# Optimization experiments

Measured on AMD Instinct MI355X. Metric: run time of the kernel, lower is better.

## Reference

```python
import jax, jax.numpy as jnp
import numpy as np

B, N, DIM, PDIM, H, DH, M, CDIM = 1, 48, 256, 128, 8, 64, 128, 512
INNER = H * DH
EPS = 1e-5


def setup_inputs() -> dict:
    key = jax.random.key(0)
    ks = jax.random.split(key, 40)
    def w(k, shape):
        return jax.random.normal(k, shape, jnp.float32) * 0.02
    inp = {
        "singles": jax.random.normal(ks[0], (B, N, DIM), jnp.float32),
        "pairs": jax.random.normal(ks[1], (B, N, N, PDIM), jnp.float32),
        "ligand_emb": jax.random.normal(ks[2], (B, M, CDIM), jnp.float32),
        "mask": jnp.ones((B, N), dtype=bool),
        "rotary_pos": jax.random.normal(ks[3], (1, 1, 1, DH), jnp.float32),
        "ln_s_g": jnp.ones((DIM,)), "ln_s_b": jnp.zeros((DIM,)),
        "ln_p_g": jnp.ones((PDIM,)), "ln_p_b": jnp.zeros((PDIM,)),
        "sa_qkv": w(ks[4], (DIM, 3 * INNER)),
        "sa_out_w": w(ks[5], (INNER, DIM)), "sa_out_b": jnp.zeros((DIM,)),
        "sff_w1": w(ks[6], (DIM, 4 * DIM)), "sff_b1": jnp.zeros((4 * DIM,)),
        "sff_w2": w(ks[7], (4 * DIM, DIM)), "sff_b2": jnp.zeros((DIM,)),
        "pa_qkv": w(ks[8], (PDIM, 3 * INNER)),
        "pa_out_w": w(ks[9], (INNER, PDIM)), "pa_out_b": jnp.zeros((PDIM,)),
        "pff_w1": w(ks[10], (PDIM, 4 * PDIM)), "pff_b1": jnp.zeros((4 * PDIM,)),
        "pff_w2": w(ks[11], (4 * PDIM, PDIM)), "pff_b2": jnp.zeros((PDIM,)),
        "ca_q": w(ks[12], (PDIM, INNER)),
        "ca_kv": w(ks[13], (CDIM, 2 * INNER)),
        "ca_out_w": w(ks[14], (INNER, PDIM)), "ca_out_b": jnp.zeros((PDIM,)),
        "s2p_w": w(ks[15], (DIM, PDIM)), "s2p_b": jnp.zeros((PDIM,)),
        "p2s_w": w(ks[16], (PDIM, DIM)), "p2s_b": jnp.zeros((DIM,)),
    }
    return inp


def _rotate_half(x):
    shp = x.shape
    xr = x.reshape(shp[:-1] + (shp[-1] // 2, 2))
    x1, x2 = xr[..., 0], xr[..., 1]
    return jnp.stack((-x2, x1), axis=-1).reshape(shp)


def _rope(pos, t):
    return t * jnp.cos(pos) + _rotate_half(t) * jnp.sin(pos)


def _split_heads(t):
    b, n, _ = t.shape
    return t.reshape(b, n, H, DH).transpose(0, 2, 1, 3)  # b h n d


def _merge_heads(t):
    b, h, n, d = t.shape
    return t.transpose(0, 2, 1, 3).reshape(b, n, h * d)


def _layer_norm(x, g, b):
    m = jnp.mean(x, axis=-1, keepdims=True)
    v = jnp.mean(jnp.square(x - m), axis=-1, keepdims=True)
    return (x - m) * jax.lax.rsqrt(v + EPS) * g + b


def _mish(x):
    return x * jnp.tanh(jax.nn.softplus(x))


def _attn_core(q, k, v, key_mask=None):
    dots = jnp.einsum('bhid,bhjd->bhij', q, k) * (DH ** -0.5)
    if key_mask is not None:
        neg = -jnp.finfo(dots.dtype).max
        dots = jnp.where(key_mask[:, None, None, :], dots, neg)
    a = jax.nn.softmax(dots, axis=-1)
    return jnp.einsum('bhij,bhjd->bhid', a, v)


def _self_attn(x, w_qkv, w_out, b_out, rotary_pos, key_mask=None):
    q, k, v = jnp.split(x @ w_qkv, 3, axis=-1)
    q, k, v = _split_heads(q), _split_heads(k), _split_heads(v)
    q, k = _rope(rotary_pos, q), _rope(rotary_pos, k)
    out = _merge_heads(_attn_core(q, k, v, key_mask))
    return out @ w_out + b_out


def _cross_attn(x, ctx, w_q, w_kv, w_out, b_out, rotary_pos):
    q = _split_heads(x @ w_q)
    k, v = jnp.split(ctx @ w_kv, 2, axis=-1)
    k, v = _split_heads(k), _split_heads(v)
    q, k = _rope(rotary_pos, q), _rope(rotary_pos, k)
    out = _merge_heads(_attn_core(q, k, v))
    return out @ w_out + b_out


def _ff(x, w1, b1, w2, b2):
    return _mish(x @ w1 + b1) @ w2 + b2


def _forward(singles, pairs, ligand_emb, mask, rotary_pos,
             ln_s_g, ln_s_b, ln_p_g, ln_p_b,
             sa_qkv, sa_out_w, sa_out_b, sff_w1, sff_b1, sff_w2, sff_b2,
             pa_qkv, pa_out_w, pa_out_b, pff_w1, pff_b1, pff_w2, pff_b2,
             ca_q, ca_kv, ca_out_w, ca_out_b, s2p_w, s2p_b, p2s_w, p2s_b):
    # single track
    s_norm = _layer_norm(singles, ln_s_g, ln_s_b)
    singles = singles + _self_attn(s_norm, sa_qkv, sa_out_w, sa_out_b, rotary_pos, mask)
    singles = singles + _ff(singles, sff_w1, sff_b1, sff_w2, sff_b2)
    # pair track: flatten i*j into one long sequence
    b, i, j, d = pairs.shape
    p_norm = _layer_norm(pairs, ln_p_g, ln_p_b)
    p_flat = p_norm.reshape(b, i * j, d)
    p_attn = _self_attn(p_flat, pa_qkv, pa_out_w, pa_out_b, rotary_pos, None)
    pairs = pairs + p_attn.reshape(b, i, j, d)
    # ligand cross attention (on pre-norm pairs, as in source)
    p_cross = _cross_attn(p_flat, ligand_emb, ca_q, ca_kv, ca_out_w, ca_out_b, rotary_pos)
    pairs = pairs + p_cross.reshape(b, i, j, d)
    pairs = pairs + _ff(pairs, pff_w1, pff_b1, pff_w2, pff_b2)
    # cross-track communication
    single_contrib = singles @ s2p_w + s2p_b              # [b,n,pdim]
    pair_contrib = jnp.mean(pairs, axis=2) @ p2s_w + p2s_b  # [b,n,dim]
    pairs = pairs + single_contrib[:, None, :, :] + single_contrib[:, :, None, :]
    singles = singles + pair_contrib
    return singles, pairs


def reference(singles, pairs, ligand_emb, mask, rotary_pos,
              ln_s_g, ln_s_b, ln_p_g, ln_p_b,
              sa_qkv, sa_out_w, sa_out_b, sff_w1, sff_b1, sff_w2, sff_b2,
              pa_qkv, pa_out_w, pa_out_b, pff_w1, pff_b1, pff_w2, pff_b2,
              ca_q, ca_kv, ca_out_w, ca_out_b, s2p_w, s2p_b, p2s_w, p2s_b):
    return _forward(singles, pairs, ligand_emb, mask, rotary_pos,
                    ln_s_g, ln_s_b, ln_p_g, ln_p_b,
                    sa_qkv, sa_out_w, sa_out_b, sff_w1, sff_b1, sff_w2, sff_b2,
                    pa_qkv, pa_out_w, pa_out_b, pff_w1, pff_b1, pff_w2, pff_b2,
                    ca_q, ca_kv, ca_out_w, ca_out_b, s2p_w, s2p_b, p2s_w, p2s_b)
```

## Files before the change

### kernel.cpp

```cpp
#include <hip/hip_runtime.h>
#include <math.h>

#define EPS 1e-5f

typedef __attribute__((ext_vector_type(8))) short short8;
typedef __attribute__((ext_vector_type(4))) short short4v;
typedef __attribute__((ext_vector_type(4))) float float4v;

__device__ inline short f2bf(float f) {
  union { float f; unsigned u; } c; c.f = f;
  unsigned u = c.u;
  u += 0x7FFF + ((u >> 16) & 1);
  return (short)(u >> 16);
}
__device__ inline float bf2f(short s) {
  union { unsigned u; float f; } c;
  c.u = ((unsigned)(unsigned short)s) << 16;
  return c.f;
}

__global__ __launch_bounds__(256) void ln_kernel(
    const float* __restrict__ xs, const float* __restrict__ gs,
    const float* __restrict__ bs, float* __restrict__ ys,
    const float* __restrict__ xp, const float* __restrict__ gp,
    const float* __restrict__ bp, float* __restrict__ yp) {
  const float *x, *g, *b;
  float* y;
  int D, row;
  if (blockIdx.x < 48) {
    row = blockIdx.x; x = xs; g = gs; b = bs; y = ys; D = 256;
  } else {
    row = blockIdx.x - 48; x = xp; g = gp; b = bp; y = yp; D = 128;
  }
  const float* xr = x + (size_t)row * D;
  float* yr = y + (size_t)row * D;
  __shared__ float red[256];
  int tid = threadIdx.x;
  float s = (tid < D) ? xr[tid] : 0.f;
  red[tid] = s; __syncthreads();
  for (int st = 128; st > 0; st >>= 1) {
    if (tid < st) red[tid] += red[tid + st];
    __syncthreads();
  }
  float mean = red[0] / D;
  __syncthreads();
  float v = 0.f;
  if (tid < D) { float t = xr[tid] - mean; v = t * t; }
  red[tid] = v; __syncthreads();
  for (int st = 128; st > 0; st >>= 1) {
    if (tid < st) red[tid] += red[tid + st];
    __syncthreads();
  }
  float rstd = rsqrtf(red[0] / D + EPS);
  if (tid < D) yr[tid] = (xr[tid] - mean) * rstd * g[tid] + b[tid];
}

struct TransDesc { const float* src; short* dst; int K; int N; int tile0; };
struct TransArgs { TransDesc d[13]; int nd; };

__global__ __launch_bounds__(256) void transpose_weights_kernel(TransArgs args) {
  int t = blockIdx.x;
  int wi = 0;
  while (wi + 1 < args.nd && args.d[wi + 1].tile0 <= t) ++wi;
  TransDesc de = args.d[wi];
  int lt = t - de.tile0;
  int ntx = de.N / 32;
  int k0 = (lt / ntx) * 32, n0 = (lt % ntx) * 32;
  __shared__ float tile[32][33];
  int tx = threadIdx.x & 31, ty = threadIdx.x >> 5;
#pragma unroll
  for (int yy = 0; yy < 4; ++yy) {
    int kk = ty + yy * 8;
    tile[kk][tx] = de.src[(size_t)(k0 + kk) * de.N + n0 + tx];
  }
  __syncthreads();
#pragma unroll
  for (int yy = 0; yy < 4; ++yy) {
    int nn = ty + yy * 8;
    de.dst[(size_t)(n0 + nn) * de.K + k0 + tx] = f2bf(tile[tx][nn]);
  }
}

struct ProjJob {
  const float* A; const short* Wt;
  int M, K, N;
  short *Qd, *Kd, *Vd;
  int rowspad, vld, qend, kend, tile0;
  float qscale;
};
struct ProjArgs { ProjJob j[4]; int nj; };

__global__ __launch_bounds__(256) void proj_kernel(
    ProjArgs args, const float* __restrict__ rope_pos) {
  __shared__ short As[64][72];
  __shared__ short Ws[64][72];
  int t = blockIdx.x;
  int ji = 0;
  while (ji + 1 < args.nj && args.j[ji + 1].tile0 <= t) ++ji;
  ProjJob jb = args.j[ji];
  int lt = t - jb.tile0;
  int ntx = jb.N / 64;
  int m0 = (lt / ntx) * 64, n0 = (lt % ntx) * 64;
  int tid = threadIdx.x;
  int wave = tid >> 6, lane = tid & 63;
  int n16 = lane & 15, quad = lane >> 4;
  float4v acc[4];
#pragma unroll
  for (int f = 0; f < 4; ++f) acc[f] = (float4v){0.f, 0.f, 0.f, 0.f};

  for (int k0 = 0; k0 < jb.K; k0 += 64) {
    __syncthreads();
    for (int idx = tid; idx < 1024; idx += 256) {
      int row = idx >> 4, c4 = (idx & 15) * 4;
      float4 av = make_float4(0.f, 0.f, 0.f, 0.f);
      if (m0 + row < jb.M)
        av = *(const float4*)(jb.A + (size_t)(m0 + row) * jb.K + k0 + c4);
      short4v s;
      s.x = f2bf(av.x); s.y = f2bf(av.y); s.z = f2bf(av.z); s.w = f2bf(av.w);
      *(short4v*)&As[row][c4] = s;
    }
    for (int idx = tid; idx < 512; idx += 256) {
      int row = idx >> 3, kc = (idx & 7) * 8;
      short8 w = *(const short8*)(jb.Wt + (size_t)(n0 + row) * jb.K + k0 + kc);
      *(short8*)&Ws[row][kc] = w;
    }
    __syncthreads();
#pragma unroll
    for (int s = 0; s < 2; ++s) {
      short8 a = *(const short8*)&As[wave * 16 + n16][s * 32 + quad * 8];
#pragma unroll
      for (int f = 0; f < 4; ++f) {
        short8 b = *(const short8*)&Ws[f * 16 + n16][s * 32 + quad * 8];
        acc[f] = __builtin_amdgcn_mfma_f32_16x16x32_bf16(a, b, acc[f], 0, 0, 0);
      }
    }
  }

#pragma unroll
  for (int f = 0; f < 4; ++f) {
    int col = n0 + f * 16 + n16;
    if (col < jb.kend) {
      int rel = (col < jb.qend) ? col : col - jb.qend;
      int hh = rel >> 6, d = col & 63;
      float pv = rope_pos[d];
      float cp = cosf(pv), sp = sinf(pv);
      float sc = (col < jb.qend) ? jb.qscale : 1.f;
      short* dst = (col < jb.qend) ? jb.Qd : jb.Kd;
#pragma unroll
      for (int r = 0; r < 4; ++r) {
        float x = acc[f][r];
        float xp = __shfl_xor(x, 1);
        float o = (n16 & 1) ? (x * cp + xp * sp) : (x * cp - xp * sp);
        int row = m0 + wave * 16 + quad * 4 + r;
        if (row < jb.M)
          dst[((size_t)hh * jb.rowspad + row) * 64 + d] = f2bf(o * sc);
      }
    } else {
      int vcol = col - jb.kend;
      int hh = vcol >> 6, d = vcol & 63;
      short4v s;
#pragma unroll
      for (int r = 0; r < 4; ++r) ((short*)&s)[r] = f2bf(acc[f][r]);
      int j0 = m0 + wave * 16 + quad * 4;
      if (j0 < jb.M)
        *(short4v*)(jb.Vd + (size_t)(hh * 64 + d) * jb.vld + j0) = s;
    }
  }
}

struct FJob {
  const short *Q, *K, *V;
  int nkpad;
  float* O;
  short* Opart; float* Lpart;
  int nq, nk, ns, nqt, blk0;
};
struct FArgs { FJob j[3]; int nj; };

__global__ __launch_bounds__(256) void fattn_kernel(FArgs args) {
  __shared__ short Ks[64][72];
  __shared__ short Vs[64][72];
  __shared__ short Ps[4][16][72];
  int bid = blockIdx.x;
  int ji = 0;
  while (ji + 1 < args.nj && args.j[ji + 1].blk0 <= bid) ++ji;
  FJob jb = args.j[ji];
  int local = bid - jb.blk0;
  int h = local & 7;
  int rest = local >> 3;
  int qt = rest % jb.nqt;
  int z = rest / jb.nqt;
  int nqpad = jb.nqt * 64;
  int q0 = qt * 64;
  int nsplit = jb.ns;
  int nkpad = jb.nkpad, nk = jb.nk;
  int tid = threadIdx.x;
  int wave = tid >> 6, lane = tid & 63;
  int n16 = lane & 15, quad = lane >> 4;

  int ntiles = nkpad >> 6;
  int tiles_per = (ntiles + nsplit - 1) / nsplit;
  int kbeg = z * tiles_per * 64;
  int kend = min(nkpad, kbeg + tiles_per * 64);

  const short* kb = jb.K + (size_t)h * nkpad * 64;
  const short* vt = jb.V + (size_t)h * 64 * nkpad;
  const short* qr = jb.Q + (size_t)h * nqpad * 64 +
                    (size_t)(q0 + wave * 16 + n16) * 64;
  short8 a0 = *(const short8*)(qr + quad * 8);
  short8 a1 = *(const short8*)(qr + 32 + quad * 8);

  float4v Of[4];
#pragma unroll
  for (int f = 0; f < 4; ++f) Of[f] = (float4v){0.f, 0.f, 0.f, 0.f};
  float l_par[4] = {0.f, 0.f, 0.f, 0.f};

  int r0 = tid >> 3, cc0 = (tid & 7) * 8;
  int r1 = (tid + 256) >> 3, cc1 = ((tid + 256) & 7) * 8;

  short8 pK0 = *(const short8*)(kb + (size_t)(kbeg + r0) * 64 + cc0);
  short8 pK1 = *(const short8*)(kb + (size_t)(kbeg + r1) * 64 + cc1);
  short8 pV0 = *(const short8*)(vt + (size_t)r0 * nkpad + kbeg + cc0);
  short8 pV1 = *(const short8*)(vt + (size_t)r1 * nkpad + kbeg + cc1);

  for (int kt0 = kbeg; kt0 < kend; kt0 += 64) {
    __syncthreads();
    *(short8*)&Ks[r0][cc0] = pK0;
    *(short8*)&Ks[r1][cc1] = pK1;
    *(short8*)&Vs[r0][cc0] = pV0;
    *(short8*)&Vs[r1][cc1] = pV1;
    int nxt = kt0 + 64;
    if (nxt < kend) {
      pK0 = *(const short8*)(kb + (size_t)(nxt + r0) * 64 + cc0);
      pK1 = *(const short8*)(kb + (size_t)(nxt + r1) * 64 + cc1);
      pV0 = *(const short8*)(vt + (size_t)r0 * nkpad + nxt + cc0);
      pV1 = *(const short8*)(vt + (size_t)r1 * nkpad + nxt + cc1);
    }
    __syncthreads();

    float4v Sf[4];
#pragma unroll
    for (int f = 0; f < 4; ++f) {
      short8 b0 = *(const short8*)&Ks[f * 16 + n16][quad * 8];
      short8 b1 = *(const short8*)&Ks[f * 16 + n16][32 + quad * 8];
      float4v a = (float4v){0.f, 0.f, 0.f, 0.f};
      a = __builtin_amdgcn_mfma_f32_16x16x32_bf16(a0, b0, a, 0, 0, 0);
      a = __builtin_amdgcn_mfma_f32_16x16x32_bf16(a1, b1, a, 0, 0, 0);
      Sf[f] = a;
    }
    if (kt0 + 64 > nk) {
#pragma unroll
      for (int f = 0; f < 4; ++f) {
        int j = kt0 + f * 16 + n16;
        if (j >= nk) {
          Sf[f][0] = -1e30f; Sf[f][1] = -1e30f;
          Sf[f][2] = -1e30f; Sf[f][3] = -1e30f;
        }
      }
    }
    float p[4][4];
#pragma unroll
    for (int r = 0; r < 4; ++r) {
      float t = 0.f;
#pragma unroll
      for (int f = 0; f < 4; ++f) {
        float e = __expf(Sf[f][r]);
        p[f][r] = e;
        t += e;
      }
      l_par[r] += t;
    }
#pragma unroll
    for (int f = 0; f < 4; ++f)
#pragma unroll
      for (int r = 0; r < 4; ++r)
        Ps[wave][quad * 4 + r][f * 16 + n16] = f2bf(p[f][r]);
#pragma unroll
    for (int s = 0; s < 2; ++s) {
      short8 pa = *(const short8*)&Ps[wave][n16][s * 32 + quad * 8];
#pragma unroll
      for (int f = 0; f < 4; ++f) {
        short8 vb = *(const short8*)&Vs[f * 16 + n16][s * 32 + quad * 8];
        Of[f] = __builtin_amdgcn_mfma_f32_16x16x32_bf16(pa, vb, Of[f], 0, 0, 0);
      }
    }
  }

  float l[4];
#pragma unroll
  for (int r = 0; r < 4; ++r) {
    float t = l_par[r];
    t += __shfl_xor(t, 1);
    t += __shfl_xor(t, 2);
    t += __shfl_xor(t, 4);
    t += __shfl_xor(t, 8);
    l[r] = t;
  }

  if (nsplit == 1) {
#pragma unroll
    for (int r = 0; r < 4; ++r) {
      int row = q0 + wave * 16 + quad * 4 + r;
      if (row >= jb.nq) continue;
      float inv = 1.f / l[r];
#pragma unroll
      for (int f = 0; f < 4; ++f)
        jb.O[(size_t)row * 512 + h * 64 + f * 16 + n16] = Of[f][r] * inv;
    }
  } else {
    size_t pbase = ((size_t)(h * jb.nqt + qt) * nsplit + z);
    short* op = jb.Opart + pbase * 4096;
#pragma unroll
    for (int r = 0; r < 4; ++r) {
      int rl = wave * 16 + quad * 4 + r;
#pragma unroll
      for (int f = 0; f < 4; ++f)
        op[(size_t)rl * 64 + f * 16 + n16] = f2bf(Of[f][r]);
      if (n16 == 0) jb.Lpart[pbase * 64 + rl] = l[r];
    }
  }
}

__global__ __launch_bounds__(256) void attn_combine_kernel(
    const short* __restrict__ Opart, const float* __restrict__ Lpart,
    float* __restrict__ O, int os, int nsplit) {
  int h = blockIdx.x, qt = blockIdx.y;
  int tid = threadIdx.x;
  int q = tid >> 2, d0 = (tid & 3) * 16;
  size_t base = (size_t)(h * gridDim.y + qt) * nsplit;
  float l = 0.f;
  for (int s = 0; s < nsplit; ++s) l += Lpart[(base + s) * 64 + q];
  float inv = 1.f / l;
  float acc[16];
#pragma unroll
  for (int i = 0; i < 16; ++i) acc[i] = 0.f;
  for (int s = 0; s < nsplit; ++s) {
    const short* op = Opart + (base + s) * 4096 + q * 64 + d0;
#pragma unroll
    for (int c = 0; c < 2; ++c) {
      short8 v = *(const short8*)(op + c * 8);
#pragma unroll
      for (int j = 0; j < 8; ++j) acc[c * 8 + j] += bf2f(v[j]);
    }
  }
  int row = qt * 64 + q;
  float* dst = O + (size_t)row * os + h * 64 + d0;
#pragma unroll
  for (int c = 0; c < 4; ++c) {
    float4 o = make_float4(acc[c * 4] * inv, acc[c * 4 + 1] * inv,
                           acc[c * 4 + 2] * inv, acc[c * 4 + 3] * inv);
    *(float4*)(dst + c * 4) = o;
  }
}

struct TJob {
  int type;
  const float *A1, *A2;
  const short *W1, *W2;
  const float *b1, *b2, *resid;
  float* C;
  int M, Kseg, N, nz, dual, mish, tile0;
};
struct TArgs { TJob j[2]; int nj; };

__global__ __launch_bounds__(256) void tjobs_kernel(TArgs args) {
  __shared__ short As[32][136];
  __shared__ short Ws[32][136];
  int t = blockIdx.x;
  int ji = 0;
  while (ji + 1 < args.nj && args.j[ji + 1].tile0 <= t) ++ji;
  TJob jb = args.j[ji];
  int lt = t - jb.tile0;
  int tid = threadIdx.x;

  if (jb.type == 1) {
    int i = lt;
    if (tid < 128) {
      float acc = 0.f;
      for (int j = 0; j < 48; ++j)
        acc += jb.A1[((size_t)i * 48 + j) * 128 + tid];
      jb.C[i * 128 + tid] = acc * (1.f / 48.f);
    }
    return;
  }
  if (jb.type == 2) {
    int idx = lt * 256 + tid;
    int d = idx & 127;
    int j = (idx >> 7) % 48;
    int i = idx / (48 * 128);
    jb.C[idx] = jb.A1[idx] + jb.A2[j * 128 + d] + jb.A2[i * 128 + d];
    return;
  }

  int ntx = jb.N / 32, nmt = (jb.M + 31) >> 5;
  int per_z = ntx * nmt;
  int z = lt / per_z, rem = lt - z * per_z;
  int m0 = (rem / ntx) * 32, n0 = (rem % ntx) * 32;
  int wave = tid >> 6, lane = tid & 63;
  int n16 = lane & 15, quad = lane >> 4;
  int mrow = (wave >> 1) * 16, ncol = (wave & 1) * 16;
  float4v acc = (float4v){0.f, 0.f, 0.f, 0.f};
  int Ktot = jb.dual ? 2 * jb.Kseg : jb.Kseg;
  int chunk = Ktot / jb.nz;
  int kst = z * chunk, ken = kst + chunk;
  for (int kc = kst; kc < ken; kc += 128) {
    __syncthreads();
    for (int idx = tid; idx < 1024; idx += 256) {
      int row = idx >> 5, c4 = (idx & 31) * 4;
      int k = kc + c4;
      float4 av = make_float4(0.f, 0.f, 0.f, 0.f);
      if (m0 + row < jb.M) {
        const float* src = (jb.dual && k >= jb.Kseg)
            ? (jb.A2 + (size_t)(m0 + row) * jb.Kseg + (k - jb.Kseg))
            : (jb.A1 + (size_t)(m0 + row) * jb.Kseg + k);
        av = *(const float4*)src;
      }
      short4v s;
      s.x = f2bf(av.x); s.y = f2bf(av.y); s.z = f2bf(av.z); s.w = f2bf(av.w);
      *(short4v*)&As[row][c4] = s;
    }
    for (int idx = tid; idx < 512; idx += 256) {
      int row = idx >> 4, k8 = (idx & 15) * 8;
      int k = kc + k8;
      const short* src = (jb.dual && k >= jb.Kseg)
          ? (jb.W2 + (size_t)(n0 + row) * jb.Kseg + (k - jb.Kseg))
          : (jb.W1 + (size_t)(n0 + row) * jb.Kseg + k);
      *(short8*)&Ws[row][k8] = *(const short8*)src;
    }
    __syncthreads();
#pragma unroll
    for (int ks = 0; ks < 4; ++ks) {
      short8 a = *(const short8*)&As[mrow + n16][ks * 32 + quad * 8];
      short8 b = *(const short8*)&Ws[ncol + n16][ks * 32 + quad * 8];
      acc = __builtin_amdgcn_mfma_f32_16x16x32_bf16(a, b, acc, 0, 0, 0);
    }
  }
  int col = n0 + ncol + n16;
  if (jb.nz == 1) {
#pragma unroll
    for (int r = 0; r < 4; ++r) {
      int row = m0 + mrow + quad * 4 + r;
      if (row >= jb.M) continue;
      float v = acc[r] + jb.b1[col];
      if (jb.dual) v += jb.b2[col];
      if (jb.mish) {
        float sp = (v > 20.f) ? v : log1pf(expf(v));
        v = v * tanhf(sp);
      }
      if (jb.resid) v += jb.resid[(size_t)row * jb.N + col];
      jb.C[(size_t)row * jb.N + col] = v;
    }
  } else {
#pragma unroll
    for (int r = 0; r < 4; ++r) {
      int row = m0 + mrow + quad * 4 + r;
      if (row >= jb.M) continue;
      float v = acc[r];
      if (z == 0) {
        v += jb.b1[col];
        if (jb.dual) v += jb.b2[col];
        if (jb.resid) v += jb.resid[(size_t)row * jb.N + col];
      }
      atomicAdd(&jb.C[(size_t)row * jb.N + col], v);
    }
  }
}

extern "C" void kernel_launch(void* const* d_in, const int* in_sizes, int n_in,
                              void* d_out, int out_size, void* d_ws, size_t ws_size,
                              hipStream_t stream) {
  (void)in_sizes; (void)n_in; (void)out_size; (void)ws_size;
  const float* singles = (const float*)d_in[0];
  const float* pairs   = (const float*)d_in[1];
  const float* ligand  = (const float*)d_in[2];
  const float* rotary  = (const float*)d_in[4];
  const float* ln_s_g  = (const float*)d_in[5];
  const float* ln_s_b  = (const float*)d_in[6];
  const float* ln_p_g  = (const float*)d_in[7];
  const float* ln_p_b  = (const float*)d_in[8];
  const float* sa_out_b= (const float*)d_in[11];
  const float* sff_b1  = (const float*)d_in[13];
  const float* sff_b2  = (const float*)d_in[15];
  const float* pa_out_b= (const float*)d_in[18];
  const float* pff_b1  = (const float*)d_in[20];
  const float* pff_b2  = (const float*)d_in[22];
  const float* ca_out_b= (const float*)d_in[26];
  const float* s2p_b   = (const float*)d_in[28];
  const float* p2s_b   = (const float*)d_in[30];

  float* ws = (float*)d_ws;
  size_t off = 0;
  auto alloc = [&](size_t n) { float* p = ws + off; off += n; return p; };
  float* s_norm   = alloc(12288);
  float* p_norm   = alloc(294912);
  float* attn_s   = alloc(24576);
  float* h1_s     = alloc(49152);
  float* attn_p   = alloc(294912);
  float* attn_c   = alloc(1179648);
  float* pairs2   = alloc(294912);
  float* pairs3   = alloc(294912);
  float* singles1 = alloc(12288);
  float* singles2 = alloc(12288);
  float* sc_buf   = alloc(6144);
  size_t zero_floats = 294912 * 2 + 12288 * 2 + 6144;
  float* pmean    = alloc(6144);
  float* Lpart    = alloc(73728);
  short* OpartS   = (short*)alloc(2359296);
  short* wt       = (short*)alloc(1081344);
  short* Qb       = (short*)alloc(589824);
  short* Kb       = (short*)alloc(589824);
  short* Vtb      = (short*)alloc(589824);
  short* Qcb      = (short*)alloc(589824);
  short* Kcb      = (short*)alloc(32768);
  short* Vcb      = (short*)alloc(32768);
  short* Qsb      = (short*)alloc(16384);
  short* Ksb      = (short*)alloc(16384);
  short* Vsb      = (short*)alloc(16384);

  float* out_s = (float*)d_out;
  float* out_p = (float*)d_out + 12288;

  struct WSpec { const float* src; int K, N; };
  WSpec specs[13] = {
    {(const float*)d_in[9], 256, 1536}, {(const float*)d_in[10], 512, 256},
    {(const float*)d_in[12], 256, 1024}, {(const float*)d_in[14], 1024, 256},
    {(const float*)d_in[16], 128, 1536}, {(const float*)d_in[17], 512, 128},
    {(const float*)d_in[19], 128, 512}, {(const float*)d_in[21], 512, 128},
    {(const float*)d_in[23], 128, 512}, {(const float*)d_in[24], 512, 1024},
    {(const float*)d_in[25], 512, 128}, {(const float*)d_in[27], 256, 128},
    {(const float*)d_in[29], 128, 256}};
  TransArgs ta;
  ta.nd = 13;
  short* wptr[13];
  int tiles = 0;
  size_t woff = 0;
  for (int i = 0; i < 13; ++i) {
    ta.d[i].src = specs[i].src;
    ta.d[i].dst = wt + woff;
    ta.d[i].K = specs[i].K;
    ta.d[i].N = specs[i].N;
    ta.d[i].tile0 = tiles;
    wptr[i] = wt + woff;
    woff += (size_t)specs[i].K * specs[i].N;
    tiles += (specs[i].K / 32) * (specs[i].N / 32);
  }
  hipLaunchKernelGGL(transpose_weights_kernel, dim3(tiles), dim3(256), 0,
                     stream, ta);
  hipMemsetAsync(pairs2, 0, zero_floats * sizeof(float), stream);

  const float scale = 0.125f;
  const int NS = 4;

  hipLaunchKernelGGL(ln_kernel, dim3(48 + 2304), dim3(256), 0, stream,
                     singles, ln_s_g, ln_s_b, s_norm,
                     pairs, ln_p_g, ln_p_b, p_norm);

  {
    ProjArgs pa;
    pa.nj = 4;
    int t0 = 0;
    auto setj = [&](int i, const float* A, const short* Wt, int M, int K,
                    int N, short* Qd, short* Kd, short* Vd, int rowspad,
                    int vld, int qend, int kend, float qscale) {
      pa.j[i] = {A, Wt, M, K, N, Qd, Kd, Vd, rowspad, vld, qend, kend, t0,
                 qscale};
      t0 += (N / 64) * ((M + 63) / 64);
    };
    setj(0, s_norm, wptr[0], 48, 256, 1536, Qsb, Ksb, Vsb, 64, 64, 512, 1024,
         scale);
    setj(1, p_norm, wptr[4], 2304, 128, 1536, Qb, Kb, Vtb, 2304, 2304, 512,
         1024, scale);
    setj(2, p_norm, wptr[8], 2304, 128, 512, Qcb, nullptr, nullptr, 2304, 0,
         512, 512, scale);
    setj(3, ligand, wptr[9], 128, 512, 1024, nullptr, Kcb, Vcb, 128, 128, 0,
         512, 1.f);
    hipLaunchKernelGGL(proj_kernel, dim3(t0), dim3(256), 0, stream, pa, rotary);
  }

  {
    FArgs fa;
    fa.nj = 3;
    fa.j[0] = {Qb, Kb, Vtb, 2304, attn_p, OpartS, Lpart, 2304, 2304, NS, 36, 0};
    fa.j[1] = {Qsb, Ksb, Vsb, 64, attn_s, nullptr, nullptr, 48, 48, 1, 1,
               8 * 36 * NS};
    fa.j[2] = {Qcb, Kcb, Vcb, 128, attn_c, nullptr, nullptr, 2304, 128, 1, 36,
               8 * 36 * NS + 8};
    int nblk = 8 * 36 * NS + 8 + 8 * 36;
    hipLaunchKernelGGL(fattn_kernel, dim3(nblk), dim3(256), 0, stream, fa);
  }

  hipLaunchKernelGGL(attn_combine_kernel, dim3(8, 36), dim3(256), 0, stream,
                     OpartS, Lpart, attn_p, 512, NS);

  auto launch_tjobs = [&](TJob a, TJob b, int nb) {
    TArgs tj;
    tj.nj = 2;
    tj.j[0] = a;
    tj.j[1] = b;
    hipLaunchKernelGGL(tjobs_kernel, dim3(nb), dim3(256), 0, stream, tj);
  };
  auto gemm_tiles = [](int M, int N, int nz) {
    return (N / 32) * ((M + 31) / 32) * nz;
  };

  {
    TJob a = {0, attn_p, attn_c, wptr[5], wptr[10], pa_out_b, ca_out_b, pairs,
              pairs2, 2304, 512, 128, 4, 1, 0, 0};
    int t1 = gemm_tiles(2304, 128, 4);
    TJob b = {0, attn_s, nullptr, wptr[1], nullptr, sa_out_b, nullptr, singles,
              singles1, 48, 512, 256, 2, 0, 0, t1};
    launch_tjobs(a, b, t1 + gemm_tiles(48, 256, 2));
  }
  {
    TJob a = {0, pairs2, nullptr, wptr[6], nullptr, pff_b1, nullptr, nullptr,
              attn_c , 2304, 128, 512, 1, 0, 1, 0};
    int t1 = gemm_tiles(2304, 512, 1);
    TJob b = {0, singles1, nullptr, wptr[2], nullptr, sff_b1, nullptr, nullptr,
              h1_s, 48, 256, 1024, 1, 0, 1, t1};
    launch_tjobs(a, b, t1 + gemm_tiles(48, 1024, 1));
  }
  {
    TJob a = {0, attn_c , nullptr, wptr[7], nullptr, pff_b2, nullptr,
              pairs2, pairs3, 2304, 512, 128, 2, 0, 0, 0};
    int t1 = gemm_tiles(2304, 128, 2);
    TJob b = {0, h1_s, nullptr, wptr[3], nullptr, sff_b2, nullptr, singles1,
              singles2, 48, 1024, 256, 2, 0, 0, t1};
    launch_tjobs(a, b, t1 + gemm_tiles(48, 256, 2));
  }
  {
    TJob a = {0, singles2, nullptr, wptr[11], nullptr, s2p_b, nullptr, nullptr,
              sc_buf, 48, 256, 128, 2, 0, 0, 0};
    int t1 = gemm_tiles(48, 128, 2);
    TJob b = {1, pairs3, nullptr, nullptr, nullptr, nullptr, nullptr, nullptr,
              pmean, 0, 0, 0, 1, 0, 0, t1};
    launch_tjobs(a, b, t1 + 48);
  }
  {
    TJob a = {0, pmean, nullptr, wptr[12], nullptr, p2s_b, nullptr, singles2,
              out_s, 48, 128, 256, 1, 0, 0, 0};
    int t1 = gemm_tiles(48, 256, 1);
    TJob b = {2, pairs3, sc_buf, nullptr, nullptr, nullptr, nullptr, nullptr,
              out_p, 0, 0, 0, 1, 0, 0, t1};
    launch_tjobs(a, b, t1 + 1152);
  }
}
```

Before: 239.4 us.

## Fuse prep kernels, replace split-K combine with atomics, fold s2p into FF

Measured after the change: 288.9 us. 20.7% more time.

```diff
diff --git a/kernel.cpp b/kernel.cpp
--- a/kernel.cpp
+++ b/kernel.cpp
@@ -13,72 +13,72 @@
   u += 0x7FFF + ((u >> 16) & 1);
   return (short)(u >> 16);
 }
-__device__ inline float bf2f(short s) {
-  union { unsigned u; float f; } c;
-  c.u = ((unsigned)(unsigned short)s) << 16;
-  return c.f;
-}
-
-__global__ __launch_bounds__(256) void ln_kernel(
+
+struct TransDesc { const float* src; short* dst; int K; int N; int tile0; };
+struct TransArgs { TransDesc d[13]; int nd; };
+
+__global__ __launch_bounds__(256) void prep_kernel(
+    TransArgs args, int tiles, int ln_end,
     const float* __restrict__ xs, const float* __restrict__ gs,
     const float* __restrict__ bs, float* __restrict__ ys,
     const float* __restrict__ xp, const float* __restrict__ gp,
-    const float* __restrict__ bp, float* __restrict__ yp) {
-  const float *x, *g, *b;
-  float* y;
-  int D, row;
-  if (blockIdx.x < 48) {
-    row = blockIdx.x; x = xs; g = gs; b = bs; y = ys; D = 256;
-  } else {
-    row = blockIdx.x - 48; x = xp; g = gp; b = bp; y = yp; D = 128;
-  }
-  const float* xr = x + (size_t)row * D;
-  float* yr = y + (size_t)row * D;
-  __shared__ float red[256];
+    const float* __restrict__ bp, float* __restrict__ yp,
+    float* __restrict__ zbase) {
+  int bid = blockIdx.x;
   int tid = threadIdx.x;
-  float s = (tid < D) ? xr[tid] : 0.f;
-  red[tid] = s; __syncthreads();
-  for (int st = 128; st > 0; st >>= 1) {
-    if (tid < st) red[tid] += red[tid + st];
-    __syncthreads();
-  }
-  float mean = red[0] / D;
-  __syncthreads();
-  float v = 0.f;
-  if (tid < D) { float t = xr[tid] - mean; v = t * t; }
-  red[tid] = v; __syncthreads();
-  for (int st = 128; st > 0; st >>= 1) {
-    if (tid < st) red[tid] += red[tid + st];
-    __syncthreads();
-  }
-  float rstd = rsqrtf(red[0] / D + EPS);
-  if (tid < D) yr[tid] = (xr[tid] - mean) * rstd * g[tid] + b[tid];
-}
-
-struct TransDesc { const float* src; short* dst; int K; int N; int tile0; };
-struct TransArgs { TransDesc d[13]; int nd; };
-
-__global__ __launch_bounds__(256) void transpose_weights_kernel(TransArgs args) {
-  int t = blockIdx.x;
-  int wi = 0;
-  while (wi + 1 < args.nd && args.d[wi + 1].tile0 <= t) ++wi;
-  TransDesc de = args.d[wi];
-  int lt = t - de.tile0;
-  int ntx = de.N / 32;
-  int k0 = (lt / ntx) * 32, n0 = (lt % ntx) * 32;
-  __shared__ float tile[32][33];
-  int tx = threadIdx.x & 31, ty = threadIdx.x >> 5;
-#pragma unroll
-  for (int yy = 0; yy < 4; ++yy) {
-    int kk = ty + yy * 8;
-    tile[kk][tx] = de.src[(size_t)(k0 + kk) * de.N + n0 + tx];
-  }
-  __syncthreads();
-#pragma unroll
-  for (int yy = 0; yy < 4; ++yy) {
-    int nn = ty + yy * 8;
-    de.dst[(size_t)(n0 + nn) * de.K + k0 + tx] = f2bf(tile[tx][nn]);
-  }
+  if (bid < tiles) {
+    __shared__ float tile[32][33];
+    int wi = 0;
+    while (wi + 1 < args.nd && args.d[wi + 1].tile0 <= bid) ++wi;
+    TransDesc de = args.d[wi];
+    int lt = bid - de.tile0;
+    int ntx = de.N / 32;
+    int k0 = (lt / ntx) * 32, n0 = (lt % ntx) * 32;
+    int tx = tid & 31, ty = tid >> 5;
+#pragma unroll
+    for (int yy = 0; yy < 4; ++yy) {
+      int kk = ty + yy * 8;
+      tile[kk][tx] = de.src[(size_t)(k0 + kk) * de.N + n0 + tx];
+    }
+    __syncthreads();
+#pragma unroll
+    for (int yy = 0; yy < 4; ++yy) {
+      int nn = ty + yy * 8;
+      de.dst[(size_t)(n0 + nn) * de.K + k0 + tx] = f2bf(tile[tx][nn]);
+    }
+    return;
+  }
+  if (bid < ln_end) {
+    __shared__ float red[256];
+    int row = bid - tiles;
+    const float *x, *g, *b;
+    float* y;
+    int D;
+    if (row < 48) { x = xs; g = gs; b = bs; y = ys; D = 256; }
+    else { row -= 48; x = xp; g = gp; b = bp; y = yp; D = 128; }
+    const float* xr = x + (size_t)row * D;
+    float* yr = y + (size_t)row * D;
+    float s = (tid < D) ? xr[tid] : 0.f;
+    red[tid] = s; __syncthreads();
+    for (int st = 128; st > 0; st >>= 1) {
+      if (tid < st) red[tid] += red[tid + st];
+      __syncthreads();
+    }
+    float mean = red[0] / D;
+    __syncthreads();
+    float v = 0.f;
+    if (tid < D) { float t = xr[tid] - mean; v = t * t; }
+    red[tid] = v; __syncthreads();
+    for (int st = 128; st > 0; st >>= 1) {
+      if (tid < st) red[tid] += red[tid + st];
+      __syncthreads();
+    }
+    float rstd = rsqrtf(red[0] / D + EPS);
+    if (tid < D) yr[tid] = (xr[tid] - mean) * rstd * g[tid] + b[tid];
+    return;
+  }
+  size_t i4 = ((size_t)(bid - ln_end) * 256 + tid) * 4;
+  *(float4*)(zbase + i4) = make_float4(0.f, 0.f, 0.f, 0.f);
 }
 
 struct ProjJob {
@@ -172,7 +172,7 @@
   const short *Q, *K, *V;
   int nkpad;
   float* O;
-  short* Opart; float* Lpart;
+  float* Lsum;
   int nq, nk, ns, nqt, blk0;
 };
 struct FArgs { FJob j[3]; int nj; };
@@ -192,14 +192,13 @@
   int z = rest / jb.nqt;
   int nqpad = jb.nqt * 64;
   int q0 = qt * 64;
-  int nsplit = jb.ns;
   int nkpad = jb.nkpad, nk = jb.nk;
   int tid = threadIdx.x;
   int wave = tid >> 6, lane = tid & 63;
   int n16 = lane & 15, quad = lane >> 4;
 
   int ntiles = nkpad >> 6;
-  int tiles_per = (ntiles + nsplit - 1) / nsplit;
+  int tiles_per = (ntiles + jb.ns - 1) / jb.ns;
   int kbeg = z * tiles_per * 64;
   int kend = min(nkpad, kbeg + tiles_per * 64);
 
@@ -297,7 +296,7 @@
     l[r] = t;
   }
 
-  if (nsplit == 1) {
+  if (jb.ns == 1) {
 #pragma unroll
     for (int r = 0; r < 4; ++r) {
       int row = q0 + wave * 16 + quad * 4 + r;
@@ -308,48 +307,14 @@
         jb.O[(size_t)row * 512 + h * 64 + f * 16 + n16] = Of[f][r] * inv;
     }
   } else {
-    size_t pbase = ((size_t)(h * jb.nqt + qt) * nsplit + z);
-    short* op = jb.Opart + pbase * 4096;
 #pragma unroll
     for (int r = 0; r < 4; ++r) {
-      int rl = wave * 16 + quad * 4 + r;
+      int row = q0 + wave * 16 + quad * 4 + r;
 #pragma unroll
       for (int f = 0; f < 4; ++f)
-        op[(size_t)rl * 64 + f * 16 + n16] = f2bf(Of[f][r]);
-      if (n16 == 0) jb.Lpart[pbase * 64 + rl] = l[r];
-    }
-  }
-}
-
-__global__ __launch_bounds__(256) void attn_combine_kernel(
-    const short* __restrict__ Opart, const float* __restrict__ Lpart,
-    float* __restrict__ O, int os, int nsplit) {
-  int h = blockIdx.x, qt = blockIdx.y;
-  int tid = threadIdx.x;
-  int q = tid >> 2, d0 = (tid & 3) * 16;
-  size_t base = (size_t)(h * gridDim.y + qt) * nsplit;
-  float l = 0.f;
-  for (int s = 0; s < nsplit; ++s) l += Lpart[(base + s) * 64 + q];
-  float inv = 1.f / l;
-  float acc[16];
-#pragma unroll
-  for (int i = 0; i < 16; ++i) acc[i] = 0.f;
-  for (int s = 0; s < nsplit; ++s) {
-    const short* op = Opart + (base + s) * 4096 + q * 64 + d0;
-#pragma unroll
-    for (int c = 0; c < 2; ++c) {
-      short8 v = *(const short8*)(op + c * 8);
-#pragma unroll
-      for (int j = 0; j < 8; ++j) acc[c * 8 + j] += bf2f(v[j]);
-    }
-  }
-  int row = qt * 64 + q;
-  float* dst = O + (size_t)row * os + h * 64 + d0;
-#pragma unroll
-  for (int c = 0; c < 4; ++c) {
-    float4 o = make_float4(acc[c * 4] * inv, acc[c * 4 + 1] * inv,
-                           acc[c * 4 + 2] * inv, acc[c * 4 + 3] * inv);
-    *(float4*)(dst + c * 4) = o;
+        atomicAdd(&jb.O[(size_t)row * 512 + h * 64 + f * 16 + n16], Of[f][r]);
+      if (n16 == 0) atomicAdd(&jb.Lsum[(size_t)h * jb.nq + row], l[r]);
+    }
   }
 }
 
@@ -357,11 +322,12 @@
   int type;
   const float *A1, *A2;
   const short *W1, *W2;
-  const float *b1, *b2, *resid;
-  float* C;
-  int M, Kseg, N, nz, dual, mish, tile0;
+  const float *b1, *b2, *resid, *normL;
+  float *C, *pmean;
+  short* Ct;
+  int M, K1, K2, N, nz, mish, dual, tile0;
 };
-struct TArgs { TJob j[2]; int nj; };
+struct TArgs { TJob j[4]; int nj; };
 
 __global__ __launch_bounds__(256) void tjobs_kernel(TArgs args) {
   __shared__ short As[32][136];
@@ -373,22 +339,21 @@
   int lt = t - jb.tile0;
   int tid = threadIdx.x;
 
-  if (jb.type == 1) {
-    int i = lt;
-    if (tid < 128) {
-      float acc = 0.f;
-      for (int j = 0; j < 48; ++j)
-        acc += jb.A1[((size_t)i * 48 + j) * 128 + tid];
-      jb.C[i * 128 + tid] = acc * (1.f / 48.f);
-    }
-    return;
-  }
   if (jb.type == 2) {
     int idx = lt * 256 + tid;
     int d = idx & 127;
     int j = (idx >> 7) % 48;
     int i = idx / (48 * 128);
     jb.C[idx] = jb.A1[idx] + jb.A2[j * 128 + d] + jb.A2[i * 128 + d];
+    return;
+  }
+  if (jb.type == 4) {
+    if (tid < 128) {
+      float acc = jb.b1[tid];
+      for (int m = 0; m < jb.K1; ++m)
+        acc += jb.A1[m] * jb.resid[(size_t)m * 128 + tid];
+      jb.C[tid] = acc;
+    }
     return;
   }
 
@@ -400,7 +365,7 @@
   int n16 = lane & 15, quad = lane >> 4;
   int mrow = (wave >> 1) * 16, ncol = (wave & 1) * 16;
   float4v acc = (float4v){0.f, 0.f, 0.f, 0.f};
-  int Ktot = jb.dual ? 2 * jb.Kseg : jb.Kseg;
+  int Ktot = jb.K1 + (jb.dual ? jb.K2 : 0);
   int chunk = Ktot / jb.nz;
   int kst = z * chunk, ken = kst + chunk;
   for (int kc = kst; kc < ken; kc += 128) {
@@ -410,10 +375,16 @@
       int k = kc + c4;
       float4 av = make_float4(0.f, 0.f, 0.f, 0.f);
       if (m0 + row < jb.M) {
-        const float* src = (jb.dual && k >= jb.Kseg)
-            ? (jb.A2 + (size_t)(m0 + row) * jb.Kseg + (k - jb.Kseg))
-            : (jb.A1 + (size_t)(m0 + row) * jb.Kseg + k);
-        av = *(const float4*)src;
+        if (!jb.dual || k < jb.K1) {
+          av = *(const float4*)(jb.A1 + (size_t)(m0 + row) * jb.K1 + k);
+          if (jb.normL) {
+            float inv = 1.f / jb.normL[(size_t)(k >> 6) * jb.M + m0 + row];
+            av.x *= inv; av.y *= inv; av.z *= inv; av.w *= inv;
+          }
+        } else {
+          av = *(const float4*)(jb.A2 + (size_t)(m0 + row) * jb.K2 +
+                                (k - jb.K1));
+        }
       }
       short4v s;
       s.x = f2bf(av.x); s.y = f2bf(av.y); s.z = f2bf(av.z); s.w = f2bf(av.w);
@@ -422,9 +393,9 @@
     for (int idx = tid; idx < 512; idx += 256) {
       int row = idx >> 4, k8 = (idx & 15) * 8;
       int k = kc + k8;
-      const short* src = (jb.dual && k >= jb.Kseg)
-          ? (jb.W2 + (size_t)(n0 + row) * jb.Kseg + (k - jb.Kseg))
-          : (jb.W1 + (size_t)(n0 + row) * jb.Kseg + k);
+      const short* src = (jb.dual && k >= jb.K1)
+          ? (jb.W2 + (size_t)(n0 + row) * jb.K2 + (k - jb.K1))
+          : (jb.W1 + (size_t)(n0 + row) * jb.K1 + k);
       *(short8*)&Ws[row][k8] = *(const short8*)src;
     }
     __syncthreads();
@@ -436,19 +407,29 @@
     }
   }
   int col = n0 + ncol + n16;
+  if (jb.Ct) {
+    short4v s;
+#pragma unroll
+    for (int r = 0; r < 4; ++r) ((short*)&s)[r] = f2bf(acc[r]);
+    int rbase = m0 + mrow + quad * 4;
+    *(short4v*)(jb.Ct + (size_t)col * jb.M + rbase) = s;
+    return;
+  }
   if (jb.nz == 1) {
 #pragma unroll
     for (int r = 0; r < 4; ++r) {
       int row = m0 + mrow + quad * 4 + r;
       if (row >= jb.M) continue;
-      float v = acc[r] + jb.b1[col];
-      if (jb.dual) v += jb.b2[col];
+      float v = acc[r];
+      if (jb.b1) v += jb.b1[col];
+      if (jb.b2) v += jb.b2[col];
       if (jb.mish) {
         float sp = (v > 20.f) ? v : log1pf(expf(v));
         v = v * tanhf(sp);
       }
       if (jb.resid) v += jb.resid[(size_t)row * jb.N + col];
       jb.C[(size_t)row * jb.N + col] = v;
+      if (jb.pmean) atomicAdd(&jb.pmean[(row / 48) * 128 + col], v * (1.f / 48.f));
     }
   } else {
 #pragma unroll
@@ -457,11 +438,12 @@
       if (row >= jb.M) continue;
       float v = acc[r];
       if (z == 0) {
-        v += jb.b1[col];
-        if (jb.dual) v += jb.b2[col];
+        if (jb.b1) v += jb.b1[col];
+        if (jb.b2) v += jb.b2[col];
         if (jb.resid) v += jb.resid[(size_t)row * jb.N + col];
       }
       atomicAdd(&jb.C[(size_t)row * jb.N + col], v);
+      if (jb.pmean) atomicAdd(&jb.pmean[(row / 48) * 128 + col], v * (1.f / 48.f));
     }
   }
 }
@@ -480,11 +462,13 @@
   const float* ln_p_b  = (const float*)d_in[8];
   const float* sa_out_b= (const float*)d_in[11];
   const float* sff_b1  = (const float*)d_in[13];
+  const float* sff_w2f = (const float*)d_in[14];
   const float* sff_b2  = (const float*)d_in[15];
   const float* pa_out_b= (const float*)d_in[18];
   const float* pff_b1  = (const float*)d_in[20];
   const float* pff_b2  = (const float*)d_in[22];
   const float* ca_out_b= (const float*)d_in[26];
+  const float* s2p_wf  = (const float*)d_in[27];
   const float* s2p_b   = (const float*)d_in[28];
   const float* p2s_b   = (const float*)d_in[30];
 
@@ -495,17 +479,18 @@
   float* p_norm   = alloc(294912);
   float* attn_s   = alloc(24576);
   float* h1_s     = alloc(49152);
-  float* attn_p   = alloc(294912);
   float* attn_c   = alloc(1179648);
+  float* attn_p   = alloc(1179648);
+  float* Lsum     = alloc(18432);
   float* pairs2   = alloc(294912);
   float* pairs3   = alloc(294912);
   float* singles1 = alloc(12288);
   float* singles2 = alloc(12288);
   float* sc_buf   = alloc(6144);
-  size_t zero_floats = 294912 * 2 + 12288 * 2 + 6144;
   float* pmean    = alloc(6144);
-  float* Lpart    = alloc(73728);
-  short* OpartS   = (short*)alloc(2359296);
+  const size_t zero_floats = 1824768;
+  float* bc       = alloc(128);
+  short* Wct      = (short*)alloc(65536);
   short* wt       = (short*)alloc(1081344);
   short* Qb       = (short*)alloc(589824);
   short* Kb       = (short*)alloc(589824);
@@ -523,11 +508,11 @@
   struct WSpec { const float* src; int K, N; };
   WSpec specs[13] = {
     {(const float*)d_in[9], 256, 1536}, {(const float*)d_in[10], 512, 256},
-    {(const float*)d_in[12], 256, 1024}, {(const float*)d_in[14], 1024, 256},
+    {(const float*)d_in[12], 256, 1024}, {sff_w2f, 1024, 256},
     {(const float*)d_in[16], 128, 1536}, {(const float*)d_in[17], 512, 128},
     {(const float*)d_in[19], 128, 512}, {(const float*)d_in[21], 512, 128},
     {(const float*)d_in[23], 128, 512}, {(const float*)d_in[24], 512, 1024},
-    {(const float*)d_in[25], 512, 128}, {(const float*)d_in[27], 256, 128},
+    {(const float*)d_in[25], 512, 128}, {s2p_wf, 256, 128},
     {(const float*)d_in[29], 128, 256}};
   TransArgs ta;
   ta.nd = 13;
@@ -544,16 +529,18 @@
     woff += (size_t)specs[i].K * specs[i].N;
     tiles += (specs[i].K / 32) * (specs[i].N / 32);
   }
-  hipLaunchKernelGGL(transpose_weights_kernel, dim3(tiles), dim3(256), 0,
-                     stream, ta);
-  hipMemsetAsync(pairs2, 0, zero_floats * sizeof(float), stream);
 
   const float scale = 0.125f;
   const int NS = 4;
 
-  hipLaunchKernelGGL(ln_kernel, dim3(48 + 2304), dim3(256), 0, stream,
-                     singles, ln_s_g, ln_s_b, s_norm,
-                     pairs, ln_p_g, ln_p_b, p_norm);
+  {
+    int ln_end = tiles + 48 + 2304;
+    int zero_blocks = (int)(zero_floats / 1024);
+    hipLaunchKernelGGL(prep_kernel, dim3(ln_end + zero_blocks), dim3(256), 0,
+                       stream, ta, tiles, ln_end,
+                       singles, ln_s_g, ln_s_b, s_norm,
+                       pairs, ln_p_g, ln_p_b, p_norm, attn_p);
+  }
 
   {
     ProjArgs pa;
@@ -580,67 +567,85 @@
   {
     FArgs fa;
     fa.nj = 3;
-    fa.j[0] = {Qb, Kb, Vtb, 2304, attn_p, OpartS, Lpart, 2304, 2304, NS, 36, 0};
-    fa.j[1] = {Qsb, Ksb, Vsb, 64, attn_s, nullptr, nullptr, 48, 48, 1, 1,
-               8 * 36 * NS};
-    fa.j[2] = {Qcb, Kcb, Vcb, 128, attn_c, nullptr, nullptr, 2304, 128, 1, 36,
+    fa.j[0] = {Qb, Kb, Vtb, 2304, attn_p, Lsum, 2304, 2304, NS, 36, 0};
+    fa.j[1] = {Qsb, Ksb, Vsb, 64, attn_s, nullptr, 48, 48, 1, 1, 8 * 36 * NS};
+    fa.j[2] = {Qcb, Kcb, Vcb, 128, attn_c, nullptr, 2304, 128, 1, 36,
                8 * 36 * NS + 8};
-    int nblk = 8 * 36 * NS + 8 + 8 * 36;
-    hipLaunchKernelGGL(fattn_kernel, dim3(nblk), dim3(256), 0, stream, fa);
-  }
-
-  hipLaunchKernelGGL(attn_combine_kernel, dim3(8, 36), dim3(256), 0, stream,
-                     OpartS, Lpart, attn_p, 512, NS);
-
-  auto launch_tjobs = [&](TJob a, TJob b, int nb) {
-    TArgs tj;
-    tj.nj = 2;
-    tj.j[0] = a;
-    tj.j[1] = b;
-    hipLaunchKernelGGL(tjobs_kernel, dim3(nb), dim3(256), 0, stream, tj);
-  };
+    hipLaunchKernelGGL(fattn_kernel, dim3(8 * 36 * NS + 8 + 8 * 36), dim3(256),
+                       0, stream, fa);
+  }
+
   auto gemm_tiles = [](int M, int N, int nz) {
     return (N / 32) * ((M + 31) / 32) * nz;
   };
+  TJob jz{};
 
   {
-    TJob a = {0, attn_p, attn_c, wptr[5], wptr[10], pa_out_b, ca_out_b, pairs,
-              pairs2, 2304, 512, 128, 4, 1, 0, 0};
+    TArgs tj; tj.nj = 4;
+    TJob a = jz;
+    a.type = 0; a.A1 = attn_p; a.A2 = attn_c; a.W1 = wptr[5]; a.W2 = wptr[10];
+    a.b1 = pa_out_b; a.b2 = ca_out_b; a.resid = pairs; a.normL = Lsum;
+    a.C = pairs2; a.M = 2304; a.K1 = 512; a.K2 = 512; a.N = 128; a.nz = 4;
+    a.dual = 1; a.tile0 = 0;
     int t1 = gemm_tiles(2304, 128, 4);
-    TJob b = {0, attn_s, nullptr, wptr[1], nullptr, sa_out_b, nullptr, singles,
-              singles1, 48, 512, 256, 2, 0, 0, t1};
-    launch_tjobs(a, b, t1 + gemm_tiles(48, 256, 2));
+    TJob b = jz;
+    b.type = 0; b.A1 = attn_s; b.W1 = wptr[1]; b.b1 = sa_out_b;
+    b.resid = singles; b.C = singles1; b.M = 48; b.K1 = 512; b.N = 256;
+    b.nz = 2; b.tile0 = t1;
+    int t2 = t1 + gemm_tiles(48, 256, 2);
+    TJob c = jz;
+    c.type = 0; c.A1 = sff_w2f; c.W1 = wptr[11]; c.Ct = Wct;
+    c.M = 1024; c.K1 = 256; c.N = 128; c.nz = 1; c.tile0 = t2;
+    int t3 = t2 + gemm_tiles(1024, 128, 1);
+    TJob d = jz;
+    d.type = 4; d.A1 = sff_b2; d.b1 = s2p_b; d.resid = s2p_wf; d.C = bc;
+    d.K1 = 256; d.tile0 = t3;
+    tj.j[0] = a; tj.j[1] = b; tj.j[2] = c; tj.j[3] = d;
+    hipLaunchKernelGGL(tjobs_kernel, dim3(t3 + 1), dim3(256), 0, stream, tj);
   }
   {
-    TJob a = {0, pairs2, nullptr, wptr[6], nullptr, pff_b1, nullptr, nullptr,
-              attn_c , 2304, 128, 512, 1, 0, 1, 0};
+    TArgs tj; tj.nj = 2;
+    TJob a = jz;
+    a.type = 0; a.A1 = pairs2; a.W1 = wptr[6]; a.b1 = pff_b1; a.mish = 1;
+    a.C = attn_c ; a.M = 2304; a.K1 = 128; a.N = 512; a.nz = 1;
+    a.tile0 = 0;
     int t1 = gemm_tiles(2304, 512, 1);
-    TJob b = {0, singles1, nullptr, wptr[2], nullptr, sff_b1, nullptr, nullptr,
-              h1_s, 48, 256, 1024, 1, 0, 1, t1};
-    launch_tjobs(a, b, t1 + gemm_tiles(48, 1024, 1));
+    TJob b = jz;
+    b.type = 0; b.A1 = singles1; b.W1 = wptr[2]; b.b1 = sff_b1; b.mish = 1;
+    b.C = h1_s; b.M = 48; b.K1 = 256; b.N = 1024; b.nz = 1; b.tile0 = t1;
+    tj.j[0] = a; tj.j[1] = b;
+    hipLaunchKernelGGL(tjobs_kernel, dim3(t1 + gemm_tiles(48, 1024, 1)),
+                       dim3(256), 0, stream, tj);
   }
   {
-    TJob a = {0, attn_c , nullptr, wptr[7], nullptr, pff_b2, nullptr,
-              pairs2, pairs3, 2304, 512, 128, 2, 0, 0, 0};
+    TArgs tj; tj.nj = 3;
+    TJob a = jz;
+    a.type = 0; a.A1 = attn_c ; a.W1 = wptr[7]; a.b1 = pff_b2;
+    a.resid = pairs2; a.C = pairs3; a.pmean = pmean;
+    a.M = 2304; a.K1 = 512; a.N = 128; a.nz = 2; a.tile0 = 0;
     int t1 = gemm_tiles(2304, 128, 2);
-    TJob b = {0, h1_s, nullptr, wptr[3], nullptr, sff_b2, nullptr, singles1,
-              singles2, 48, 1024, 256, 2, 0, 0, t1};
-    launch_tjobs(a, b, t1 + gemm_tiles(48, 256, 2));
+    TJob b = jz;
+    b.type = 0; b.A1 = h1_s; b.W1 = wptr[3]; b.b1 = sff_b2; b.resid = singles1;
+    b.C = singles2; b.M = 48; b.K1 = 1024; b.N = 256; b.nz = 2; b.tile0 = t1;
+    int t2 = t1 + gemm_tiles(48, 256, 2);
+    TJob c = jz;
+    c.type = 0; c.A1 = singles1; c.A2 = h1_s; c.W1 = wptr[11]; c.W2 = Wct;
+    c.b1 = bc; c.C = sc_buf; c.M = 48; c.K1 = 256; c.K2 = 1024; c.N = 128;
+    c.nz = 2; c.dual = 1; c.tile0 = t2;
+    tj.j[0] = a; tj.j[1] = b; tj.j[2] = c;
+    hipLaunchKernelGGL(tjobs_kernel, dim3(t2 + gemm_tiles(48, 128, 2)),
+                       dim3(256), 0, stream, tj);
   }
   {
-    TJob a = {0, singles2, nullptr, wptr[11], nullptr, s2p_b, nullptr, nullptr,
-              sc_buf, 48, 256, 128, 2, 0, 0, 0};
-    int t1 = gemm_tiles(48, 128, 2);
-    TJob b = {1, pairs3, nullptr, nullptr, nullptr, nullptr, nullptr, nullptr,
-              pmean, 0, 0, 0, 1, 0, 0, t1};
-    launch_tjobs(a, b, t1 + 48);
-  }
-  {
-    TJob a = {0, pmean, nullptr, wptr[12], nullptr, p2s_b, nullptr, singles2,
-              out_s, 48, 128, 256, 1, 0, 0, 0};
+    TArgs tj; tj.nj = 2;
+    TJob a = jz;
+    a.type = 0; a.A1 = pmean; a.W1 = wptr[12]; a.b1 = p2s_b;
+    a.resid = singles2; a.C = out_s; a.M = 48; a.K1 = 128; a.N = 256;
+    a.nz = 1; a.tile0 = 0;
     int t1 = gemm_tiles(48, 256, 1);
-    TJob b = {2, pairs3, sc_buf, nullptr, nullptr, nullptr, nullptr, nullptr,
-              out_p, 0, 0, 0, 1, 0, 0, t1};
-    launch_tjobs(a, b, t1 + 1152);
+    TJob b = jz;
+    b.type = 2; b.A1 = pairs3; b.A2 = sc_buf; b.C = out_p; b.tile0 = t1;
+    tj.j[0] = a; tj.j[1] = b;
+    hipLaunchKernelGGL(tjobs_kernel, dim3(t1 + 1152), dim3(256), 0, stream, tj);
   }
 }
```
